# Kernel tuning notes

Measured on AMD Instinct MI355X. Metric: run time of the kernel, lower is better.

The kernel has to match this reference:

```python
import jax, jax.numpy as jnp
import numpy as np

# Topology constants (fixed DAG ontology)
B = 16384          # batch
IN_DIM = 4096      # input_dim
N_LEAF = 64        # leaf terms with direct input maps
IPL = 64           # inputs per leaf (disjoint slices; one-hot connection mask -> diag weights)
N_MID = 16         # mid-level modules
CPM = 4            # leaf children per mid module
MID_N = 128        # neurons per mid module
OUT = 256          # output_dim at root


def setup_inputs() -> dict:
    key = jax.random.key(0)
    k = jax.random.split(key, 7)
    return {
        "x": jax.random.normal(k[0], (B, IN_DIM), jnp.float32),
        # input-layer kernels: only the masked diagonal entries of each [IN_DIM, IPL]
        # kernel are nonzero after kernel*connections, so store them as [N_LEAF, IPL]
        "w_inp": jax.random.normal(k[1], (N_LEAF, IPL), jnp.float32) * 0.1,
        "pbias": jnp.ones((N_LEAF,), jnp.float32),  # pbias=1.0 per input layer
        "W_mid": jax.random.normal(k[2], (N_MID, CPM * IPL, MID_N), jnp.float32) * 0.05,
        "b_mid": jnp.zeros((N_MID, MID_N), jnp.float32),
        "W_root": jax.random.normal(k[3], (N_MID * MID_N, OUT), jnp.float32) * 0.05,
        "b_root": jnp.zeros((OUT,), jnp.float32),
    }


def reference(x, w_inp, pbias, W_mid, b_mid, W_root, b_root):
    b = x.shape[0]
    # Leaf input layers: gather each leaf's input slice, multiply by its diagonal
    # kernel entries (== dot(x, kernel*one_hot_mask)), linear act, add pbias.
    leaf = x.reshape(b, N_LEAF, IPL) * w_inp + pbias[:, None]          # [B, N_LEAF, IPL]
    # Mid modules: concat CPM leaf children -> masked-dense (mask all ones) + bias + tanh
    mid_in = leaf.reshape(b, N_MID, CPM * IPL)                          # [B, N_MID, 256]
    mid = jnp.tanh(jnp.einsum('bgi,gio->bgo', mid_in, W_mid) + b_mid)   # [B, N_MID, 128]
    # Root module: concat all mid children -> dense + bias, linear output activation
    out = mid.reshape(b, N_MID * MID_N) @ W_root + b_root               # [B, OUT]
    return out
```

## Files before the change

kernel.cpp:

```cpp
#include <hip/hip_runtime.h>

typedef __attribute__((ext_vector_type(8))) short short8;
typedef __attribute__((ext_vector_type(4))) float floatx4;
typedef unsigned short ushort_t;
typedef unsigned int uint32;


__device__ __forceinline__ uint32 f2bf_bits(float f) {
  uint32 u = __builtin_bit_cast(uint32, f);
  u += 0x7fffu + ((u >> 16) & 1u);
  return u >> 16;
}

__device__ __forceinline__ float tanh_fast(float x) {
  float e = __expf(2.0f * x);
  return 1.0f - 2.0f * __builtin_amdgcn_rcpf(e + 1.0f);
}

__device__ __forceinline__ void gl_lds16(const void* g, void* l) {
  __builtin_amdgcn_global_load_lds((const __attribute__((address_space(1))) void*)g,
                                   (__attribute__((address_space(3))) void*)l,
                                   16, 0, 0);
}


__global__ __launch_bounds__(256) void prep(const float* __restrict__ w_inp,
                                            const float* __restrict__ pbias,
                                            const float* __restrict__ W_mid,
                                            const float* __restrict__ b_mid,
                                            const float* __restrict__ W_root,
                                            ushort_t* __restrict__ Wtm,
                                            ushort_t* __restrict__ Wtr,
                                            float* __restrict__ bias_eff) {
  const int b = blockIdx.x, t = threadIdx.x;
  if (b < 2048) {
    const int idx = b * 256 + t;
    const int g = idx >> 15;
    const int rem = idx & 32767;
    const int i = rem >> 7;
    const int o = rem & 127;
    const float v = W_mid[(g << 15) + i * 128 + o] * w_inp[g * 256 + i];
    Wtm[(g << 15) + o * 256 + i] = (ushort_t)f2bf_bits(v);
  } else if (b < 4096) {
    const int idx = (b - 2048) * 256 + t;
    const int k = idx >> 8;
    const int o = idx & 255;
    Wtr[o * 2048 + k] = (ushort_t)f2bf_bits(W_root[k * 256 + o]);
  } else {
    const int g = b - 4096;
    const int o = t;
    if (o < 128) {
      float s = b_mid[g * 128 + o];
      const float* wp = W_mid + (g << 15) + o;
      float pb[4];
#pragma unroll
      for (int q = 0; q < 4; ++q) pb[q] = pbias[g * 4 + q];
#pragma unroll 8
      for (int i = 0; i < 256; ++i) s += pb[i >> 6] * wp[i * 128];
      bias_eff[g * 128 + o] = s;
    }
  }
}


__global__ __launch_bounds__(256) void midk(const float* __restrict__ x,
                                            const ushort_t* __restrict__ Wtm,
                                            const float* __restrict__ bias_eff,
                                            ushort_t* __restrict__ mid) {
  __shared__ __align__(16) unsigned char smem[34816];
  ushort_t* sA = (ushort_t*)smem;
  ushort_t* sB = (ushort_t*)(smem + 10240);

  const int t = threadIdx.x;
  const int lane = t & 63;
  const int wv = __builtin_amdgcn_readfirstlane(t >> 6);
  const int g = blockIdx.y;
  const int m0 = blockIdx.x * 128;

  const int wm = (wv & 1) * 64;
  const int wn = (wv >> 1) * 64;

  const int ar = t >> 1, ah = t & 1;
  const float* agp = x + (m0 + ar) * 4096 + g * 256 + ah * 16;
  ushort_t* asw = sA + ar * 40 + ah * 16;

  const ushort_t* bgp = Wtm + (g << 15) + (wv * 32 + (lane >> 2)) * 256 + (lane & 3) * 8;
  ushort_t* bl = sB + (wv * 32) * 32;

  floatx4 acc[4][4] = {};

  for (int kk = 0; kk < 8; ++kk) {
    __syncthreads();
    gl_lds16(bgp + kk * 32, bl);
    gl_lds16(bgp + 16 * 256 + kk * 32, bl + 16 * 32);

    const float4* ap4 = (const float4*)(agp + kk * 32);
    float4 f0 = ap4[0], f1 = ap4[1], f2 = ap4[2], f3 = ap4[3];
    uint32 u0 = f2bf_bits(f0.x) | (f2bf_bits(f0.y) << 16);
    uint32 u1 = f2bf_bits(f0.z) | (f2bf_bits(f0.w) << 16);
    uint32 u2 = f2bf_bits(f1.x) | (f2bf_bits(f1.y) << 16);
    uint32 u3 = f2bf_bits(f1.z) | (f2bf_bits(f1.w) << 16);
    uint32 u4 = f2bf_bits(f2.x) | (f2bf_bits(f2.y) << 16);
    uint32 u5 = f2bf_bits(f2.z) | (f2bf_bits(f2.w) << 16);
    uint32 u6 = f2bf_bits(f3.x) | (f2bf_bits(f3.y) << 16);
    uint32 u7 = f2bf_bits(f3.z) | (f2bf_bits(f3.w) << 16);
    ((uint4*)asw)[0] = make_uint4(u0, u1, u2, u3);
    ((uint4*)asw)[1] = make_uint4(u4, u5, u6, u7);
    __syncthreads();

    short8 af[4], bfrag[4];
#pragma unroll
    for (int mi = 0; mi < 4; ++mi)
      af[mi] = *(const short8*)(sA + (wm + mi * 16 + (lane & 15)) * 40 + (lane >> 4) * 8);
#pragma unroll
    for (int ni = 0; ni < 4; ++ni)
      bfrag[ni] = *(const short8*)(sB + (wn + ni * 16 + (lane & 15)) * 32 + (lane >> 4) * 8);
#pragma unroll
    for (int mi = 0; mi < 4; ++mi)
#pragma unroll
      for (int ni = 0; ni < 4; ++ni)
        acc[mi][ni] = __builtin_amdgcn_mfma_f32_16x16x32_bf16(af[mi], bfrag[ni], acc[mi][ni], 0, 0, 0);
  }

  __syncthreads();
  ushort_t* sC = (ushort_t*)smem;
#pragma unroll
  for (int ni = 0; ni < 4; ++ni) {
    const int col = wn + ni * 16 + (lane & 15);
    const float bias = bias_eff[g * 128 + col];
#pragma unroll
    for (int mi = 0; mi < 4; ++mi) {
#pragma unroll
      for (int r = 0; r < 4; ++r) {
        const int row = wm + mi * 16 + (lane >> 4) * 4 + r;
        sC[row * 136 + col] = (ushort_t)f2bf_bits(tanh_fast(acc[mi][ni][r] + bias));
      }
    }
  }
  __syncthreads();
  const int rr = t >> 1, hh = t & 1;
  const uint4* src = (const uint4*)(sC + rr * 136 + hh * 64);
  uint4* dst = (uint4*)(mid + (m0 + rr) * 2048 + g * 128 + hh * 64);
#pragma unroll
  for (int i = 0; i < 8; ++i) dst[i] = src[i];
}


__global__ __launch_bounds__(256) void rootk(const ushort_t* __restrict__ mid,
                                             const ushort_t* __restrict__ Wtr,
                                             float* __restrict__ partial) {
  __shared__ __align__(16) ushort_t sA[128 * 32];
  __shared__ __align__(16) ushort_t sB[128 * 32];

  const int t = threadIdx.x;
  const int lane = t & 63;
  const int wv = __builtin_amdgcn_readfirstlane(t >> 6);
  const int m0 = blockIdx.x * 128;
  const int n0 = blockIdx.y * 128;
  const int kz = blockIdx.z;

  const int wm = (wv & 1) * 64;
  const int wn = (wv >> 1) * 64;

  const ushort_t* ag = mid + (m0 + wv * 32 + (lane >> 2)) * 2048 + kz * 1024 + (lane & 3) * 8;
  const ushort_t* bg = Wtr + (n0 + wv * 32 + (lane >> 2)) * 2048 + kz * 1024 + (lane & 3) * 8;
  ushort_t* al = sA + (wv * 32) * 32;
  ushort_t* bl = sB + (wv * 32) * 32;

  floatx4 acc[4][4] = {};

  for (int kk = 0; kk < 32; ++kk) {
    __syncthreads();
    gl_lds16(ag + kk * 32, al);
    gl_lds16(ag + 16 * 2048 + kk * 32, al + 16 * 32);
    gl_lds16(bg + kk * 32, bl);
    gl_lds16(bg + 16 * 2048 + kk * 32, bl + 16 * 32);
    __syncthreads();

    short8 af[4], bfrag[4];
#pragma unroll
    for (int mi = 0; mi < 4; ++mi)
      af[mi] = *(const short8*)(sA + (wm + mi * 16 + (lane & 15)) * 32 + (lane >> 4) * 8);
#pragma unroll
    for (int ni = 0; ni < 4; ++ni)
      bfrag[ni] = *(const short8*)(sB + (wn + ni * 16 + (lane & 15)) * 32 + (lane >> 4) * 8);
#pragma unroll
    for (int mi = 0; mi < 4; ++mi)
#pragma unroll
      for (int ni = 0; ni < 4; ++ni)
        acc[mi][ni] = __builtin_amdgcn_mfma_f32_16x16x32_bf16(af[mi], bfrag[ni], acc[mi][ni], 0, 0, 0);
  }

  float* pout = partial + (size_t)kz * (16384 * 256);
#pragma unroll
  for (int ni = 0; ni < 4; ++ni) {
    const int col = n0 + wn + ni * 16 + (lane & 15);
#pragma unroll
    for (int mi = 0; mi < 4; ++mi)
#pragma unroll
      for (int r = 0; r < 4; ++r) {
        const int row = m0 + wm + mi * 16 + (lane >> 4) * 4 + r;
        pout[row * 256 + col] = acc[mi][ni][r];
      }
  }
}


__global__ __launch_bounds__(256) void reducek(const float* __restrict__ partial,
                                               const float* __restrict__ b_root,
                                               float* __restrict__ out) {
  const int i4 = (blockIdx.x * 256 + threadIdx.x) * 4;
  float4 a = *(const float4*)(partial + i4);
  float4 b = *(const float4*)(partial + (16384 * 256) + i4);
  float4 c = *(const float4*)(b_root + (i4 & 255));
  float4 r = make_float4(a.x + b.x + c.x, a.y + b.y + c.y,
                         a.z + b.z + c.z, a.w + b.w + c.w);
  *(float4*)(out + i4) = r;
}


extern "C" void kernel_launch(void* const* d_in, const int* in_sizes, int n_in,
                              void* d_out, int out_size, void* d_ws, size_t ws_size,
                              hipStream_t stream) {
  const float* x      = (const float*)d_in[0];
  const float* w_inp  = (const float*)d_in[1];
  const float* pbias  = (const float*)d_in[2];
  const float* W_mid  = (const float*)d_in[3];
  const float* b_mid  = (const float*)d_in[4];
  const float* W_root = (const float*)d_in[5];
  const float* b_root = (const float*)d_in[6];
  float* out = (float*)d_out;

  char* ws = (char*)d_ws;
  ushort_t* Wtm      = (ushort_t*)(ws);
  ushort_t* Wtr      = (ushort_t*)(ws + (1 << 20));
  float*    bias_eff = (float*)   (ws + (2 << 20));
  ushort_t* midbuf   = (ushort_t*)(ws + (4 << 20));
  float*    partials = (float*)   (ws + (72u << 20));

  prep<<<dim3(4112), dim3(256), 0, stream>>>(w_inp, pbias, W_mid, b_mid, W_root, Wtm, Wtr, bias_eff);
  midk<<<dim3(128, 16), dim3(256), 0, stream>>>(x, Wtm, bias_eff, midbuf);
  rootk<<<dim3(128, 2, 2), dim3(256), 0, stream>>>(midbuf, Wtr, partials);
  reducek<<<dim3(4096), dim3(256), 0, stream>>>(partials, b_root, out);
}
```

Measured before the change: 463.2 us.

## Fuse mid and root GEMMs into one kernel keeping mid activations in LDS

```diff
diff --git a/kernel.cpp b/kernel.cpp
--- a/kernel.cpp
+++ b/kernel.cpp
@@ -17,11 +17,7 @@
   return 1.0f - 2.0f * __builtin_amdgcn_rcpf(e + 1.0f);
 }
 
-__device__ __forceinline__ void gl_lds16(const void* g, void* l) {
-  __builtin_amdgcn_global_load_lds((const __attribute__((address_space(1))) void*)g,
-                                   (__attribute__((address_space(3))) void*)l,
-                                   16, 0, 0);
-}
+#define MFMA16(a, b, c) __builtin_amdgcn_mfma_f32_16x16x32_bf16((a), (b), (c), 0, 0, 0)
 
 
 __global__ __launch_bounds__(256) void prep(const float* __restrict__ w_inp,
@@ -63,159 +59,144 @@
 }
 
 
-__global__ __launch_bounds__(256) void midk(const float* __restrict__ x,
-                                            const ushort_t* __restrict__ Wtm,
-                                            const float* __restrict__ bias_eff,
-                                            ushort_t* __restrict__ mid) {
-  __shared__ __align__(16) unsigned char smem[34816];
-  ushort_t* sA = (ushort_t*)smem;
-  ushort_t* sB = (ushort_t*)(smem + 10240);
+__global__ __launch_bounds__(256) void fused(const float* __restrict__ x,
+                                             const ushort_t* __restrict__ Wtm,
+                                             const ushort_t* __restrict__ Wtr,
+                                             const float* __restrict__ bias_eff,
+                                             const float* __restrict__ b_root,
+                                             float* __restrict__ out) {
+  __shared__ __align__(16) ushort_t sX[32 * 264];
+  __shared__ __align__(16) ushort_t sMid[32 * 136];
 
   const int t = threadIdx.x;
   const int lane = t & 63;
   const int wv = __builtin_amdgcn_readfirstlane(t >> 6);
-  const int g = blockIdx.y;
-  const int m0 = blockIdx.x * 128;
-
-  const int wm = (wv & 1) * 64;
-  const int wn = (wv >> 1) * 64;
-
-  const int ar = t >> 1, ah = t & 1;
-  const float* agp = x + (m0 + ar) * 4096 + g * 256 + ah * 16;
-  ushort_t* asw = sA + ar * 40 + ah * 16;
-
-  const ushort_t* bgp = Wtm + (g << 15) + (wv * 32 + (lane >> 2)) * 256 + (lane & 3) * 8;
-  ushort_t* bl = sB + (wv * 32) * 32;
-
-  floatx4 acc[4][4] = {};
-
-  for (int kk = 0; kk < 8; ++kk) {
+  const int m0 = blockIdx.x * 32;
+  const int l15 = lane & 15;
+  const int kh = lane >> 4;
+
+  const int xr = t >> 3, xq = t & 7;
+  const float* xbase = x + (size_t)(m0 + xr) * 4096 + xq * 4;
+  uint32* sxw = (uint32*)(sX + xr * 264 + xq * 4);
+
+  const ushort_t* sxa0 = sX + l15 * 264 + kh * 8;
+  const ushort_t* sxa1 = sX + (16 + l15) * 264 + kh * 8;
+  const ushort_t* sma0 = sMid + l15 * 136 + kh * 8;
+  const ushort_t* sma1 = sMid + (16 + l15) * 136 + kh * 8;
+
+  const ushort_t* wtm_b0 = Wtm + (wv * 32 + l15) * 256 + kh * 8;
+  const ushort_t* wtm_b1 = Wtm + (wv * 32 + 16 + l15) * 256 + kh * 8;
+  const ushort_t* wtr_b  = Wtr + (wv * 64 + l15) * 2048 + kh * 8;
+
+  float4 rx[8];
+  floatx4 racc[2][4] = {};
+
+#pragma unroll
+  for (int p = 0; p < 8; ++p) rx[p] = *(const float4*)(xbase + p * 32);
+
+  for (int g = 0; g < 16; ++g) {
     __syncthreads();
-    gl_lds16(bgp + kk * 32, bl);
-    gl_lds16(bgp + 16 * 256 + kk * 32, bl + 16 * 32);
-
-    const float4* ap4 = (const float4*)(agp + kk * 32);
-    float4 f0 = ap4[0], f1 = ap4[1], f2 = ap4[2], f3 = ap4[3];
-    uint32 u0 = f2bf_bits(f0.x) | (f2bf_bits(f0.y) << 16);
-    uint32 u1 = f2bf_bits(f0.z) | (f2bf_bits(f0.w) << 16);
-    uint32 u2 = f2bf_bits(f1.x) | (f2bf_bits(f1.y) << 16);
-    uint32 u3 = f2bf_bits(f1.z) | (f2bf_bits(f1.w) << 16);
-    uint32 u4 = f2bf_bits(f2.x) | (f2bf_bits(f2.y) << 16);
-    uint32 u5 = f2bf_bits(f2.z) | (f2bf_bits(f2.w) << 16);
-    uint32 u6 = f2bf_bits(f3.x) | (f2bf_bits(f3.y) << 16);
-    uint32 u7 = f2bf_bits(f3.z) | (f2bf_bits(f3.w) << 16);
-    ((uint4*)asw)[0] = make_uint4(u0, u1, u2, u3);
-    ((uint4*)asw)[1] = make_uint4(u4, u5, u6, u7);
+
+#pragma unroll
+    for (int p = 0; p < 8; ++p) {
+      uint32 bx = __builtin_bit_cast(uint32, rx[p].x) + 0x8000u;
+      uint32 by = __builtin_bit_cast(uint32, rx[p].y) + 0x8000u;
+      uint32 bz = __builtin_bit_cast(uint32, rx[p].z) + 0x8000u;
+      uint32 bw = __builtin_bit_cast(uint32, rx[p].w) + 0x8000u;
+      uint32 lo = __builtin_amdgcn_perm(by, bx, 0x07060302u);
+      uint32 hi = __builtin_amdgcn_perm(bw, bz, 0x07060302u);
+      *(uint2*)(sxw + p * 16) = make_uint2(lo, hi);
+    }
+
+    const ushort_t* wb0 = wtm_b0 + (g << 15);
+    const ushort_t* wb1 = wtm_b1 + (g << 15);
+    short8 mb[2][2];
+    mb[0][0] = *(const short8*)(wb0);
+    mb[0][1] = *(const short8*)(wb1);
+    mb[1][0] = *(const short8*)(wb0 + 32);
+    mb[1][1] = *(const short8*)(wb1 + 32);
+
+    {
+      const float* xn = xbase + (g < 15 ? g + 1 : 15) * 256;
+#pragma unroll
+      for (int p = 0; p < 8; ++p) rx[p] = *(const float4*)(xn + p * 32);
+    }
+
+    const float bias0 = bias_eff[g * 128 + wv * 32 + l15];
+    const float bias1 = bias_eff[g * 128 + wv * 32 + 16 + l15];
+
     __syncthreads();
 
-    short8 af[4], bfrag[4];
-#pragma unroll
-    for (int mi = 0; mi < 4; ++mi)
-      af[mi] = *(const short8*)(sA + (wm + mi * 16 + (lane & 15)) * 40 + (lane >> 4) * 8);
-#pragma unroll
-    for (int ni = 0; ni < 4; ++ni)
-      bfrag[ni] = *(const short8*)(sB + (wn + ni * 16 + (lane & 15)) * 32 + (lane >> 4) * 8);
-#pragma unroll
-    for (int mi = 0; mi < 4; ++mi)
+    floatx4 macc[2][2] = {};
+#pragma unroll
+    for (int kk = 0; kk < 8; ++kk) {
+      short8 a0 = *(const short8*)(sxa0 + kk * 32);
+      short8 a1 = *(const short8*)(sxa1 + kk * 32);
+      short8 b0 = mb[kk & 1][0], b1 = mb[kk & 1][1];
+      const int kn = (kk + 2 <= 7) ? kk + 2 : 7;
+      mb[kk & 1][0] = *(const short8*)(wb0 + kn * 32);
+      mb[kk & 1][1] = *(const short8*)(wb1 + kn * 32);
+      macc[0][0] = MFMA16(a0, b0, macc[0][0]);
+      macc[0][1] = MFMA16(a0, b1, macc[0][1]);
+      macc[1][0] = MFMA16(a1, b0, macc[1][0]);
+      macc[1][1] = MFMA16(a1, b1, macc[1][1]);
+    }
+
+#pragma unroll
+    for (int ni = 0; ni < 2; ++ni) {
+      const float bias = ni ? bias1 : bias0;
+      const int col = wv * 32 + ni * 16 + l15;
+#pragma unroll
+      for (int mi = 0; mi < 2; ++mi)
+#pragma unroll
+        for (int r = 0; r < 4; ++r) {
+          const int row = mi * 16 + kh * 4 + r;
+          sMid[row * 136 + col] = (ushort_t)f2bf_bits(tanh_fast(macc[mi][ni][r] + bias));
+        }
+    }
+
+    const ushort_t* wb = wtr_b + g * 128;
+    short8 rb[2][4];
+#pragma unroll
+    for (int ni = 0; ni < 4; ++ni) rb[0][ni] = *(const short8*)(wb + ni * 16 * 2048);
+#pragma unroll
+    for (int ni = 0; ni < 4; ++ni) rb[1][ni] = *(const short8*)(wb + ni * 16 * 2048 + 32);
+
+    __syncthreads();
+
+#pragma unroll
+    for (int kk2 = 0; kk2 < 4; ++kk2) {
+      short8 a0 = *(const short8*)(sma0 + kk2 * 32);
+      short8 a1 = *(const short8*)(sma1 + kk2 * 32);
+      short8 b0 = rb[kk2 & 1][0], b1 = rb[kk2 & 1][1];
+      short8 b2 = rb[kk2 & 1][2], b3 = rb[kk2 & 1][3];
+      const int kn = (kk2 + 2 <= 3) ? kk2 + 2 : 3;
 #pragma unroll
       for (int ni = 0; ni < 4; ++ni)
-        acc[mi][ni] = __builtin_amdgcn_mfma_f32_16x16x32_bf16(af[mi], bfrag[ni], acc[mi][ni], 0, 0, 0);
+        rb[kk2 & 1][ni] = *(const short8*)(wb + ni * 16 * 2048 + kn * 32);
+      racc[0][0] = MFMA16(a0, b0, racc[0][0]);
+      racc[0][1] = MFMA16(a0, b1, racc[0][1]);
+      racc[0][2] = MFMA16(a0, b2, racc[0][2]);
+      racc[0][3] = MFMA16(a0, b3, racc[0][3]);
+      racc[1][0] = MFMA16(a1, b0, racc[1][0]);
+      racc[1][1] = MFMA16(a1, b1, racc[1][1]);
+      racc[1][2] = MFMA16(a1, b2, racc[1][2]);
+      racc[1][3] = MFMA16(a1, b3, racc[1][3]);
+    }
   }
 
-  __syncthreads();
-  ushort_t* sC = (ushort_t*)smem;
 #pragma unroll
   for (int ni = 0; ni < 4; ++ni) {
-    const int col = wn + ni * 16 + (lane & 15);
-    const float bias = bias_eff[g * 128 + col];
-#pragma unroll
-    for (int mi = 0; mi < 4; ++mi) {
+    const int col = wv * 64 + ni * 16 + l15;
+    const float br = b_root[col];
+#pragma unroll
+    for (int mi = 0; mi < 2; ++mi)
 #pragma unroll
       for (int r = 0; r < 4; ++r) {
-        const int row = wm + mi * 16 + (lane >> 4) * 4 + r;
-        sC[row * 136 + col] = (ushort_t)f2bf_bits(tanh_fast(acc[mi][ni][r] + bias));
-      }
-    }
-  }
-  __syncthreads();
-  const int rr = t >> 1, hh = t & 1;
-  const uint4* src = (const uint4*)(sC + rr * 136 + hh * 64);
-  uint4* dst = (uint4*)(mid + (m0 + rr) * 2048 + g * 128 + hh * 64);
-#pragma unroll
-  for (int i = 0; i < 8; ++i) dst[i] = src[i];
-}
-
-
-__global__ __launch_bounds__(256) void rootk(const ushort_t* __restrict__ mid,
-                                             const ushort_t* __restrict__ Wtr,
-                                             float* __restrict__ partial) {
-  __shared__ __align__(16) ushort_t sA[128 * 32];
-  __shared__ __align__(16) ushort_t sB[128 * 32];
-
-  const int t = threadIdx.x;
-  const int lane = t & 63;
-  const int wv = __builtin_amdgcn_readfirstlane(t >> 6);
-  const int m0 = blockIdx.x * 128;
-  const int n0 = blockIdx.y * 128;
-  const int kz = blockIdx.z;
-
-  const int wm = (wv & 1) * 64;
-  const int wn = (wv >> 1) * 64;
-
-  const ushort_t* ag = mid + (m0 + wv * 32 + (lane >> 2)) * 2048 + kz * 1024 + (lane & 3) * 8;
-  const ushort_t* bg = Wtr + (n0 + wv * 32 + (lane >> 2)) * 2048 + kz * 1024 + (lane & 3) * 8;
-  ushort_t* al = sA + (wv * 32) * 32;
-  ushort_t* bl = sB + (wv * 32) * 32;
-
-  floatx4 acc[4][4] = {};
-
-  for (int kk = 0; kk < 32; ++kk) {
-    __syncthreads();
-    gl_lds16(ag + kk * 32, al);
-    gl_lds16(ag + 16 * 2048 + kk * 32, al + 16 * 32);
-    gl_lds16(bg + kk * 32, bl);
-    gl_lds16(bg + 16 * 2048 + kk * 32, bl + 16 * 32);
-    __syncthreads();
-
-    short8 af[4], bfrag[4];
-#pragma unroll
-    for (int mi = 0; mi < 4; ++mi)
-      af[mi] = *(const short8*)(sA + (wm + mi * 16 + (lane & 15)) * 32 + (lane >> 4) * 8);
-#pragma unroll
-    for (int ni = 0; ni < 4; ++ni)
-      bfrag[ni] = *(const short8*)(sB + (wn + ni * 16 + (lane & 15)) * 32 + (lane >> 4) * 8);
-#pragma unroll
-    for (int mi = 0; mi < 4; ++mi)
-#pragma unroll
-      for (int ni = 0; ni < 4; ++ni)
-        acc[mi][ni] = __builtin_amdgcn_mfma_f32_16x16x32_bf16(af[mi], bfrag[ni], acc[mi][ni], 0, 0, 0);
-  }
-
-  float* pout = partial + (size_t)kz * (16384 * 256);
-#pragma unroll
-  for (int ni = 0; ni < 4; ++ni) {
-    const int col = n0 + wn + ni * 16 + (lane & 15);
-#pragma unroll
-    for (int mi = 0; mi < 4; ++mi)
-#pragma unroll
-      for (int r = 0; r < 4; ++r) {
-        const int row = m0 + wm + mi * 16 + (lane >> 4) * 4 + r;
-        pout[row * 256 + col] = acc[mi][ni][r];
+        const int row = m0 + mi * 16 + kh * 4 + r;
+        out[row * 256 + col] = racc[mi][ni][r] + br;
       }
   }
-}
-
-
-__global__ __launch_bounds__(256) void reducek(const float* __restrict__ partial,
-                                               const float* __restrict__ b_root,
-                                               float* __restrict__ out) {
-  const int i4 = (blockIdx.x * 256 + threadIdx.x) * 4;
-  float4 a = *(const float4*)(partial + i4);
-  float4 b = *(const float4*)(partial + (16384 * 256) + i4);
-  float4 c = *(const float4*)(b_root + (i4 & 255));
-  float4 r = make_float4(a.x + b.x + c.x, a.y + b.y + c.y,
-                         a.z + b.z + c.z, a.w + b.w + c.w);
-  *(float4*)(out + i4) = r;
 }
 
 
@@ -235,11 +216,7 @@
   ushort_t* Wtm      = (ushort_t*)(ws);
   ushort_t* Wtr      = (ushort_t*)(ws + (1 << 20));
   float*    bias_eff = (float*)   (ws + (2 << 20));
-  ushort_t* midbuf   = (ushort_t*)(ws + (4 << 20));
-  float*    partials = (float*)   (ws + (72u << 20));
 
   prep<<<dim3(4112), dim3(256), 0, stream>>>(w_inp, pbias, W_mid, b_mid, W_root, Wtm, Wtr, bias_eff);
-  midk<<<dim3(128, 16), dim3(256), 0, stream>>>(x, Wtm, bias_eff, midbuf);
-  rootk<<<dim3(128, 2, 2), dim3(256), 0, stream>>>(midbuf, Wtr, partials);
-  reducek<<<dim3(4096), dim3(256), 0, stream>>>(partials, b_root, out);
-}
+  fused<<<dim3(512), dim3(256), 0, stream>>>(x, Wtm, Wtr, bias_eff, b_root, out);
+}
```

New measurement: 452.2 us. 2.4% less time.
